# Kernel tuning notes

Hardware: AMD Instinct MI355X
Metric: run time of the kernel (lower is better)

## Reference

```python
import math
import jax, jax.numpy as jnp
import numpy as np

DIM = 512
HEADS = 8
HEAD_DIM = DIM // HEADS


def get_slopes(n):
    def pow2(n):
        start = 2 ** (-2 ** (-(math.log2(n) - 3)))
        return [start * start ** i for i in range(n)]
    if math.log2(n).is_integer():
        return pow2(n)
    c = 2 ** math.floor(math.log2(n))
    return pow2(c) + get_slopes(2 * c)[0::2][: n - c]


def setup_inputs() -> dict:
    key = jax.random.key(0)
    ks = jax.random.split(key, 12)
    b, n, d = 2, 4096, DIM
    s = 1.0 / math.sqrt(d)
    inp = {
        "x": jax.random.normal(ks[0], (b, n, d), jnp.float32),
        # coords in a ~[0,100) spatial range (tile grid coordinates)
        "coords": jax.random.uniform(ks[1], (b, n, 2), jnp.float32) * 100.0,
        "Wq": jax.random.normal(ks[2], (d, d), jnp.float32) * s,
        "bq": jnp.zeros((d,), jnp.float32),
        "Wk": jax.random.normal(ks[3], (d, d), jnp.float32) * s,
        "bk": jnp.zeros((d,), jnp.float32),
        "Wv": jax.random.normal(ks[4], (d, d), jnp.float32) * s,
        "bv": jnp.zeros((d,), jnp.float32),
        "Wp": jax.random.normal(ks[5], (d, d), jnp.float32) * s,
        "bp": jnp.zeros((d,), jnp.float32),
        "slopes": jnp.asarray(get_slopes(HEADS), jnp.float32),  # [h]
    }
    return inp


def reference(x, coords, Wq, bq, Wk, bk, Wv, bv, Wp, bp, slopes):
    b, n_q, d = x.shape
    h, hd = HEADS, HEAD_DIM
    # self-attention: context = x, context_coords = coords
    q = (x @ Wq + bq).reshape(b, n_q, h, hd).transpose(0, 2, 1, 3)  # b h nq hd
    k = (x @ Wk + bk).reshape(b, n_q, h, hd).transpose(0, 2, 1, 3)
    v = (x @ Wv + bv).reshape(b, n_q, h, hd).transpose(0, 2, 1, 3)
    # Euclidean-distance ALiBi bias: [b, h, nq, nk]
    diff = coords[:, :, None, :] - coords[:, None, :, :]          # b nq nk 2
    dist = jnp.sqrt(jnp.sum(diff * diff, axis=-1))                # b nq nk
    bias = -slopes[None, :, None, None] * dist[:, None, :, :]     # b h nq nk
    scores = jnp.einsum("bhqd,bhkd->bhqk", q, k) / math.sqrt(hd) + bias
    attn = jax.nn.softmax(scores, axis=-1)
    out = jnp.einsum("bhqk,bhkd->bhqd", attn, v)
    out = out.transpose(0, 2, 1, 3).reshape(b, n_q, d)
    return out @ Wp + bp
```

## Files before the change

### kernel.cpp

```cpp
#include <hip/hip_runtime.h>
#include <stdint.h>

typedef __bf16 bf16;
typedef __attribute__((ext_vector_type(8))) __bf16 bf16x8;
typedef __attribute__((ext_vector_type(4))) __bf16 bf16x4;
typedef __attribute__((ext_vector_type(4))) float f32x4;

#define DEVFN static __device__ __forceinline__

DEVFN void gload16(const bf16* g, char* l) {
  __builtin_amdgcn_global_load_lds(
      (const __attribute__((address_space(1))) void*)g,
      (__attribute__((address_space(3))) void*)l, 16, 0, 0);
}
DEVFN void gload4(const float* g, char* l) {
  __builtin_amdgcn_global_load_lds(
      (const __attribute__((address_space(1))) void*)g,
      (__attribute__((address_space(3))) void*)l, 4, 0, 0);
}

DEVFN int swz(int row, int kb) { return row * 128 + (kb ^ ((row & 7) << 4)); }

#define PS 9437184LL

__global__ __launch_bounds__(256) void prep_kernel(
    const float* __restrict__ x, const float* __restrict__ Wq,
    const float* __restrict__ Wk, const float* __restrict__ Wv,
    const float* __restrict__ Wp, bf16* __restrict__ xb,
    bf16* __restrict__ Wt, bf16* __restrict__ Wpt) {
  const int64_t tid = blockIdx.x * 256LL + threadIdx.x;
  const int64_t stride = (int64_t)gridDim.x * 256LL;
  for (int64_t i = tid; i < (8192LL * 512) / 4; i += stride) {
    float4 v = ((const float4*)x)[i];
    bf16x4 o = {(bf16)v.x, (bf16)v.y, (bf16)v.z, (bf16)v.w};
    ((bf16x4*)xb)[i] = o;
  }
  for (int64_t i = tid; i < 1536LL * 512; i += stride) {
    int c = (int)(i >> 9), k = (int)(i & 511);
    int wsel = c >> 9, cc = c & 511;
    const float* W = wsel == 0 ? Wq : (wsel == 1 ? Wk : Wv);
    Wt[i] = (bf16)W[k * 512 + cc];
  }
  for (int64_t i = tid; i < 512LL * 512; i += stride) {
    int c = (int)(i >> 9), k = (int)(i & 511);
    Wpt[i] = (bf16)Wp[k * 512 + c];
  }
}

DEVFN void gemm_main(const bf16* __restrict__ A, const bf16* __restrict__ B,
                     int rowA0, int rowB0, char* sA, char* sB, f32x4 acc[4][4],
                     int wr, int wc, int lane, int w) {
#pragma unroll
  for (int m = 0; m < 4; m++)
#pragma unroll
    for (int n = 0; n < 4; n++) acc[m][n] = (f32x4){0.f, 0.f, 0.f, 0.f};
  const int lr = lane >> 3;
  const int kswz = 8 * ((lane & 7) ^ lr);
  for (int k0 = 0; k0 < 512; k0 += 64) {
#pragma unroll
    for (int j = 0; j < 4; j++) {
      const int c = w * 4 + j;
      gload16(A + (rowA0 + c * 8 + lr) * 512 + k0 + kswz, sA + c * 1024);
      gload16(B + (rowB0 + c * 8 + lr) * 512 + k0 + kswz, sB + c * 1024);
    }
    __syncthreads();
    bf16x8 af[4][2], bfv[4][2];
#pragma unroll
    for (int m = 0; m < 4; m++)
#pragma unroll
      for (int kk = 0; kk < 2; kk++) {
        af[m][kk] = *(const bf16x8*)(sA + swz(wr * 64 + m * 16 + (lane & 15),
                                              kk * 64 + (lane >> 4) * 16));
        bfv[m][kk] = *(const bf16x8*)(sB + swz(wc * 64 + m * 16 + (lane & 15),
                                               kk * 64 + (lane >> 4) * 16));
      }
#pragma unroll
    for (int m = 0; m < 4; m++)
#pragma unroll
      for (int n = 0; n < 4; n++)
#pragma unroll
        for (int kk = 0; kk < 2; kk++)
          acc[m][n] = __builtin_amdgcn_mfma_f32_16x16x32_bf16(
              af[m][kk], bfv[n][kk], acc[m][n], 0, 0, 0);
    __syncthreads();
  }
}

__global__ __launch_bounds__(256) void qkv_gemm(
    const bf16* __restrict__ xb, const bf16* __restrict__ Wt,
    const float* __restrict__ bq, const float* __restrict__ bk,
    const float* __restrict__ bv, bf16* __restrict__ Qb, bf16* __restrict__ Kb,
    bf16* __restrict__ Vt) {
  __shared__ __align__(128) char sA[16384];
  __shared__ __align__(128) char sB[16384];
  const int lane = threadIdx.x & 63, w = threadIdx.x >> 6;
  const int wr = w >> 1, wc = w & 1;
  const int rowA0 = blockIdx.y * 128;
  const int colB0 = blockIdx.x * 128;
  f32x4 acc[4][4];
  gemm_main(xb, Wt, rowA0, colB0, sA, sB, acc, wr, wc, lane, w);
  const int which = colB0 >> 9;
  const int cc0 = colB0 & 511;
  const float* bias = which == 0 ? bq : (which == 1 ? bk : bv);
  const float QSCALE = 0.18033688011112042f;
#pragma unroll
  for (int m = 0; m < 4; m++)
#pragma unroll
    for (int n = 0; n < 4; n++)
#pragma unroll
      for (int r = 0; r < 4; r++) {
        int row = rowA0 + wr * 64 + m * 16 + (lane >> 4) * 4 + r;
        int col = cc0 + wc * 64 + n * 16 + (lane & 15);
        float v = acc[m][n][r] + bias[col];
        if (which == 0) {
          Qb[(int64_t)row * 512 + col] = (bf16)(v * QSCALE);
        } else if (which == 1) {
          Kb[(int64_t)row * 512 + col] = (bf16)v;
        } else {
          int b = row >> 12, nn = row & 4095;
          int hh = col >> 6, e = col & 63;
          Vt[(((int64_t)(b * 8 + hh)) * 64 + e) * 4096 + nn] = (bf16)v;
        }
      }
}

__global__ __launch_bounds__(256) void out_gemm(const bf16* __restrict__ Ob,
                                                const bf16* __restrict__ Wpt,
                                                const float* __restrict__ bp,
                                                float* __restrict__ out) {
  __shared__ __align__(128) char sA[16384];
  __shared__ __align__(128) char sB[16384];
  const int lane = threadIdx.x & 63, w = threadIdx.x >> 6;
  const int wr = w >> 1, wc = w & 1;
  const int rowA0 = blockIdx.y * 128;
  const int colB0 = blockIdx.x * 128;
  f32x4 acc[4][4];
  gemm_main(Ob, Wpt, rowA0, colB0, sA, sB, acc, wr, wc, lane, w);
#pragma unroll
  for (int m = 0; m < 4; m++)
#pragma unroll
    for (int n = 0; n < 4; n++)
#pragma unroll
      for (int r = 0; r < 4; r++) {
        int row = rowA0 + wr * 64 + m * 16 + (lane >> 4) * 4 + r;
        int col = colB0 + wc * 64 + n * 16 + (lane & 15);
        out[(int64_t)row * 512 + col] = acc[m][n][r] + bp[col];
      }
}

__global__ __launch_bounds__(512) void attn_kernel(
    const bf16* __restrict__ Qb, const bf16* __restrict__ Kb,
    const bf16* __restrict__ Vt, const float* __restrict__ coords,
    const float* __restrict__ slopes, char* __restrict__ part) {
  __shared__ __align__(128) char sK[2 * 8192];
  __shared__ __align__(128) char sV[2 * 8192];
  __shared__ __align__(128) char sC[2 * 512];
  __shared__ __align__(128) char sP[8 * 2048];

  const int tid = threadIdx.x;
  const int lane = tid & 63, w = tid >> 6;
  const int c = lane & 15, g = lane >> 4;

  const int id = blockIdx.x;
  const int bh = id & 15;
  const int qt = (id >> 4) & 31;
  const int ks = id >> 9;
  const int b = bh >> 3, h = bh & 7;
  const int qw = qt * 128 + w * 16;
  const int bO = b * 4096;
  const int kvs = ks * 2048;

  const float LOG2E = 1.4426950408889634f;
  const float negsl2 = -slopes[h] * LOG2E;

  bf16x8 aq[2];
  {
    int64_t base = ((int64_t)(bO + qw + c)) * 512 + h * 64 + g * 8;
    aq[0] = *(const bf16x8*)(Qb + base);
    aq[1] = *(const bf16x8*)(Qb + base + 32);
  }
  const float* cbf = coords + (int64_t)bO * 2;
  float qcx, qcy;
  {
    float2 qc = ((const float2*)cbf)[qw + c];
    qcx = qc.x;
    qcy = qc.y;
  }

  bf16x8 ones;
#pragma unroll
  for (int jj = 0; jj < 8; jj++) ones[jj] = (bf16)1.0f;

  float m2 = -1e30f;
  f32x4 o[4], osum;
#pragma unroll
  for (int n = 0; n < 4; n++) o[n] = (f32x4){0.f, 0.f, 0.f, 0.f};
  osum = (f32x4){0.f, 0.f, 0.f, 0.f};

  const bf16* Kp = Kb + (int64_t)bO * 512 + h * 64;
  const bf16* Vp = Vt + (int64_t)(b * 8 + h) * 262144;

  const int gi = w * 64 + lane;
  const int kr = gi >> 3, kj = gi & 7;
  const bf16* kq =
      Kp + (int64_t)(kvs + kr) * 512 + ((kj ^ (kr & 7)) * 8);
  const bf16* vq = Vp + kr * 4096 + kvs + ((kj ^ (kr & 7)) * 8);
  const float* cq = cbf + kvs * 2 + (w & 1) * 64 + lane;

  auto STAGE = [&](int bb) {
    gload16(kq, sK + bb * 8192 + gi * 16);
    kq += 64 * 512;
    gload16(vq, sV + bb * 8192 + gi * 16);
    vq += 64;
    if (w == 2 || w == 3) {
      gload4(cq, sC + bb * 512 + (w & 1) * 256);
      cq += 128;
    }
  };

  STAGE(0);
  __syncthreads();

  char* pwv = sP + w * 2048;
  const int cm = c & 7;
  for (int tt = 0; tt < 32; ++tt) {
    const int bb = tt & 1;
    if (tt + 1 < 32) STAGE(bb ^ 1);

    const char* kb = sK + bb * 8192;
    const char* vb = sV + bb * 8192;
    const char* cb0 = sC + bb * 512;

    bf16x8 kf[4][2];
#pragma unroll
    for (int t = 0; t < 4; t++)
#pragma unroll
      for (int kk = 0; kk < 2; kk++)
        kf[t][kk] = *(const bf16x8*)(kb + (t * 16 + c) * 128 +
                                     (((kk * 4 + g) ^ cm) * 16));
    float s[4][4];
    __builtin_amdgcn_s_setprio(1);
#pragma unroll
    for (int t = 0; t < 4; t++) {
      f32x4 sa = (f32x4){0.f, 0.f, 0.f, 0.f};
      sa = __builtin_amdgcn_mfma_f32_16x16x32_bf16(kf[t][0], aq[0], sa, 0, 0, 0);
      sa = __builtin_amdgcn_mfma_f32_16x16x32_bf16(kf[t][1], aq[1], sa, 0, 0, 0);
#pragma unroll
      for (int r = 0; r < 4; r++) s[t][r] = sa[r];
    }
    __builtin_amdgcn_s_setprio(0);

#pragma unroll
    for (int t = 0; t < 4; t++) {
      f32x4 ca = *(const f32x4*)(cb0 + 128 * t + 32 * g);
      f32x4 cb2 = *(const f32x4*)(cb0 + 128 * t + 32 * g + 16);
      float dx, dy;
#define DIST1(T, R, CX, CY)                                              \
  dx = qcx - (CX);                                                       \
  dy = qcy - (CY);                                                       \
  s[T][R] = __builtin_fmaf(__builtin_amdgcn_sqrtf(dx * dx + dy * dy),    \
                           negsl2, s[T][R]);
      DIST1(t, 0, ca[0], ca[1])
      DIST1(t, 1, ca[2], ca[3])
      DIST1(t, 2, cb2[0], cb2[1])
      DIST1(t, 3, cb2[2], cb2[3])
#undef DIST1
    }

    float lm = fmaxf(fmaxf(fmaxf(s[0][0], s[0][1]), fmaxf(s[0][2], s[0][3])),
                     fmaxf(fmaxf(s[1][0], s[1][1]), fmaxf(s[1][2], s[1][3])));
    lm = fmaxf(lm,
               fmaxf(fmaxf(fmaxf(s[2][0], s[2][1]), fmaxf(s[2][2], s[2][3])),
                     fmaxf(fmaxf(s[3][0], s[3][1]), fmaxf(s[3][2], s[3][3]))));
    if (__any(lm > m2 + 8.f)) {
      float lmf = fmaxf(lm, __shfl_xor(lm, 16));
      lmf = fmaxf(lmf, __shfl_xor(lmf, 32));
      float nm = fmaxf(m2, lmf);
      float sc = __builtin_amdgcn_exp2f(m2 - nm);
      m2 = nm;
      float scr[4];
#pragma unroll
      for (int r = 0; r < 4; r++)
        scr[r] = __shfl(sc, (lane & 48) | (4 * g + r));
#pragma unroll
      for (int n = 0; n < 4; n++)
#pragma unroll
        for (int r = 0; r < 4; r++) o[n][r] *= scr[r];
#pragma unroll
      for (int r = 0; r < 4; r++) osum[r] *= scr[r];
    }

#pragma unroll
    for (int t = 0; t < 4; t++) {
      bf16x4 pv = {(bf16)__builtin_amdgcn_exp2f(s[t][0] - m2),
                   (bf16)__builtin_amdgcn_exp2f(s[t][1] - m2),
                   (bf16)__builtin_amdgcn_exp2f(s[t][2] - m2),
                   (bf16)__builtin_amdgcn_exp2f(s[t][3] - m2)};
      *(bf16x4*)(pwv + c * 128 + (((2 * t + (g >> 1)) ^ cm) * 16) +
                 (g & 1) * 8) = pv;
    }
    bf16x8 pa0 = *(const bf16x8*)(pwv + c * 128 + ((g ^ cm) * 16));
    bf16x8 pa1 = *(const bf16x8*)(pwv + c * 128 + (((4 + g) ^ cm) * 16));

    __builtin_amdgcn_s_setprio(1);
#pragma unroll
    for (int n = 0; n < 4; n++) {
      const int e = n * 16 + c;
      bf16x8 vf0 = *(const bf16x8*)(vb + e * 128 + ((g ^ (e & 7)) * 16));
      bf16x8 vf1 = *(const bf16x8*)(vb + e * 128 + (((4 + g) ^ (e & 7)) * 16));
      o[n] = __builtin_amdgcn_mfma_f32_16x16x32_bf16(pa0, vf0, o[n], 0, 0, 0);
      o[n] = __builtin_amdgcn_mfma_f32_16x16x32_bf16(pa1, vf1, o[n], 0, 0, 0);
    }
    osum = __builtin_amdgcn_mfma_f32_16x16x32_bf16(pa0, ones, osum, 0, 0, 0);
    osum = __builtin_amdgcn_mfma_f32_16x16x32_bf16(pa1, ones, osum, 0, 0, 0);
    __builtin_amdgcn_s_setprio(0);

    __syncthreads();
  }

  float m2r[4];
#pragma unroll
  for (int r = 0; r < 4; r++)
    m2r[r] = __shfl(m2, (lane & 48) | (4 * g + r));
  char* pb0 = part + ks * PS + ((int64_t)bh * 4096 + qw) * 144;
#pragma unroll
  for (int r = 0; r < 4; r++) {
    char* pb = pb0 + (g * 4 + r) * 144;
    if (c == 0) {
      *(float*)pb = m2r[r];
      *((float*)pb + 1) = osum[r];
    }
#pragma unroll
    for (int n = 0; n < 4; n++)
      *(bf16*)(pb + 16 + (n * 16 + c) * 2) = (bf16)o[n][r];
  }
}

__global__ __launch_bounds__(256) void combine_kernel(
    const char* __restrict__ part, bf16* __restrict__ Ob) {
  const int t = blockIdx.x * 256 + threadIdx.x;
  const int row = t >> 6;
  const int e = t & 63;
  const char* p0 = part + (int64_t)row * 144;
  const char* p1 = p0 + PS;
  const float m0 = *(const float*)p0, s0 = *((const float*)p0 + 1);
  const float m1 = *(const float*)p1, s1 = *((const float*)p1 + 1);
  const float o0 = (float)*(const bf16*)(p0 + 16 + e * 2);
  const float o1 = (float)*(const bf16*)(p1 + 16 + e * 2);
  const float m = fmaxf(m0, m1);
  const float w0 = __builtin_amdgcn_exp2f(m0 - m);
  const float w1 = __builtin_amdgcn_exp2f(m1 - m);
  const float res = (o0 * w0 + o1 * w1) / (s0 * w0 + s1 * w1);
  const int bh = row >> 12, q = row & 4095;
  Ob[((int64_t)((bh >> 3) * 4096 + q)) * 512 + (bh & 7) * 64 + e] = (bf16)res;
}

extern "C" void kernel_launch(void* const* d_in, const int* in_sizes, int n_in,
                              void* d_out, int out_size, void* d_ws,
                              size_t ws_size, hipStream_t stream) {
  const float* x = (const float*)d_in[0];
  const float* coords = (const float*)d_in[1];
  const float* Wq = (const float*)d_in[2];
  const float* bq = (const float*)d_in[3];
  const float* Wk = (const float*)d_in[4];
  const float* bk = (const float*)d_in[5];
  const float* Wv = (const float*)d_in[6];
  const float* bv = (const float*)d_in[7];
  const float* Wp = (const float*)d_in[8];
  const float* bp = (const float*)d_in[9];
  const float* slopes = (const float*)d_in[10];

  char* ws = (char*)d_ws;
  bf16* xb = (bf16*)(ws);
  bf16* Wt = (bf16*)(ws + 8388608);
  bf16* Wpt = (bf16*)(ws + 9961472);
  bf16* Qb = (bf16*)(ws + 10485760);
  bf16* Kb = (bf16*)(ws + 18874368);
  bf16* Vt = (bf16*)(ws + 27262976);
  bf16* Ob = (bf16*)(ws + 35651584);
  char* part = ws + 44040192;

  hipLaunchKernelGGL(prep_kernel, dim3(1024), dim3(256), 0, stream, x, Wq, Wk,
                     Wv, Wp, xb, Wt, Wpt);
  hipLaunchKernelGGL(qkv_gemm, dim3(12, 64), dim3(256), 0, stream, xb, Wt, bq,
                     bk, bv, Qb, Kb, Vt);
  hipLaunchKernelGGL(attn_kernel, dim3(1024), dim3(512), 0, stream, Qb, Kb,
                     Vt, coords, slopes, part);
  hipLaunchKernelGGL(combine_kernel, dim3(16384), dim3(256), 0, stream, part,
                     Ob);
  hipLaunchKernelGGL(out_gemm, dim3(4, 64), dim3(256), 0, stream, Ob, Wpt, bp,
                     (float*)d_out);
}
```

Measured before the change: 215.1 us.

## Process two 16-row query sub-tiles per wave to reuse K/V fragments

Each wave now handles 32 query rows (two 16-row sub-tiles) instead of 16, so every K and V fragment loaded from LDS feeds twice as many MFMAs, and each block covers 256 queries. The grid is halved to 512 blocks, which cuts K/V global traffic and staging per query. In exchange, register pressure roughly doubles for accumulators and scores, and fewer blocks (512 on a GPU with 256 CUs) may reduce occupancy and latency hiding. The per-wave P scratch buffer is reused serially for both sub-tiles, which adds an LDS write/read dependency.

```diff
diff --git a/kernel.cpp b/kernel.cpp
--- a/kernel.cpp
+++ b/kernel.cpp
@@ -163,47 +163,49 @@
 
   const int id = blockIdx.x;
   const int bh = id & 15;
-  const int qt = (id >> 4) & 31;
-  const int ks = id >> 9;
+  const int qt = (id >> 4) & 15;
+  const int ks = id >> 8;
   const int b = bh >> 3, h = bh & 7;
-  const int qw = qt * 128 + w * 16;
+  const int qw = qt * 256 + w * 32;
   const int bO = b * 4096;
   const int kvs = ks * 2048;
 
   const float LOG2E = 1.4426950408889634f;
   const float negsl2 = -slopes[h] * LOG2E;
 
-  bf16x8 aq[2];
-  {
-    int64_t base = ((int64_t)(bO + qw + c)) * 512 + h * 64 + g * 8;
-    aq[0] = *(const bf16x8*)(Qb + base);
-    aq[1] = *(const bf16x8*)(Qb + base + 32);
-  }
+  bf16x8 aq[2][2];
+  float qcx[2], qcy[2];
   const float* cbf = coords + (int64_t)bO * 2;
-  float qcx, qcy;
-  {
-    float2 qc = ((const float2*)cbf)[qw + c];
-    qcx = qc.x;
-    qcy = qc.y;
+#pragma unroll
+  for (int s2 = 0; s2 < 2; s2++) {
+    int64_t base =
+        ((int64_t)(bO + qw + s2 * 16 + c)) * 512 + h * 64 + g * 8;
+    aq[s2][0] = *(const bf16x8*)(Qb + base);
+    aq[s2][1] = *(const bf16x8*)(Qb + base + 32);
+    float2 qc = ((const float2*)cbf)[qw + s2 * 16 + c];
+    qcx[s2] = qc.x;
+    qcy[s2] = qc.y;
   }
 
   bf16x8 ones;
 #pragma unroll
   for (int jj = 0; jj < 8; jj++) ones[jj] = (bf16)1.0f;
 
-  float m2 = -1e30f;
-  f32x4 o[4], osum;
-#pragma unroll
-  for (int n = 0; n < 4; n++) o[n] = (f32x4){0.f, 0.f, 0.f, 0.f};
-  osum = (f32x4){0.f, 0.f, 0.f, 0.f};
+  float m2[2] = {-1e30f, -1e30f};
+  f32x4 o[2][4], osum[2];
+#pragma unroll
+  for (int s2 = 0; s2 < 2; s2++) {
+#pragma unroll
+    for (int n = 0; n < 4; n++) o[s2][n] = (f32x4){0.f, 0.f, 0.f, 0.f};
+    osum[s2] = (f32x4){0.f, 0.f, 0.f, 0.f};
+  }
 
   const bf16* Kp = Kb + (int64_t)bO * 512 + h * 64;
   const bf16* Vp = Vt + (int64_t)(b * 8 + h) * 262144;
 
   const int gi = w * 64 + lane;
   const int kr = gi >> 3, kj = gi & 7;
-  const bf16* kq =
-      Kp + (int64_t)(kvs + kr) * 512 + ((kj ^ (kr & 7)) * 8);
+  const bf16* kq = Kp + (int64_t)(kvs + kr) * 512 + ((kj ^ (kr & 7)) * 8);
   const bf16* vq = Vp + kr * 4096 + kvs + ((kj ^ (kr & 7)) * 8);
   const float* cq = cbf + kvs * 2 + (w & 1) * 64 + lane;
 
@@ -238,69 +240,81 @@
       for (int kk = 0; kk < 2; kk++)
         kf[t][kk] = *(const bf16x8*)(kb + (t * 16 + c) * 128 +
                                      (((kk * 4 + g) ^ cm) * 16));
-    float s[4][4];
+    float s[2][4][4];
     __builtin_amdgcn_s_setprio(1);
 #pragma unroll
-    for (int t = 0; t < 4; t++) {
-      f32x4 sa = (f32x4){0.f, 0.f, 0.f, 0.f};
-      sa = __builtin_amdgcn_mfma_f32_16x16x32_bf16(kf[t][0], aq[0], sa, 0, 0, 0);
-      sa = __builtin_amdgcn_mfma_f32_16x16x32_bf16(kf[t][1], aq[1], sa, 0, 0, 0);
-#pragma unroll
-      for (int r = 0; r < 4; r++) s[t][r] = sa[r];
-    }
+    for (int s2 = 0; s2 < 2; s2++)
+#pragma unroll
+      for (int t = 0; t < 4; t++) {
+        f32x4 sa = (f32x4){0.f, 0.f, 0.f, 0.f};
+        sa = __builtin_amdgcn_mfma_f32_16x16x32_bf16(kf[t][0], aq[s2][0], sa,
+                                                     0, 0, 0);
+        sa = __builtin_amdgcn_mfma_f32_16x16x32_bf16(kf[t][1], aq[s2][1], sa,
+                                                     0, 0, 0);
+#pragma unroll
+        for (int r = 0; r < 4; r++) s[s2][t][r] = sa[r];
+      }
     __builtin_amdgcn_s_setprio(0);
 
-#pragma unroll
-    for (int t = 0; t < 4; t++) {
-      f32x4 ca = *(const f32x4*)(cb0 + 128 * t + 32 * g);
-      f32x4 cb2 = *(const f32x4*)(cb0 + 128 * t + 32 * g + 16);
-      float dx, dy;
-#define DIST1(T, R, CX, CY)                                              \
-  dx = qcx - (CX);                                                       \
-  dy = qcy - (CY);                                                       \
-  s[T][R] = __builtin_fmaf(__builtin_amdgcn_sqrtf(dx * dx + dy * dy),    \
-                           negsl2, s[T][R]);
-      DIST1(t, 0, ca[0], ca[1])
-      DIST1(t, 1, ca[2], ca[3])
-      DIST1(t, 2, cb2[0], cb2[1])
-      DIST1(t, 3, cb2[2], cb2[3])
+    bf16x8 pa[2][2];
+#pragma unroll
+    for (int s2 = 0; s2 < 2; s2++) {
+#pragma unroll
+      for (int t = 0; t < 4; t++) {
+        f32x4 ca = *(const f32x4*)(cb0 + 128 * t + 32 * g);
+        f32x4 cb2 = *(const f32x4*)(cb0 + 128 * t + 32 * g + 16);
+        float dx, dy;
+#define DIST1(T, R, CX, CY)                                                \
+  dx = qcx[s2] - (CX);                                                     \
+  dy = qcy[s2] - (CY);                                                     \
+  s[s2][T][R] = __builtin_fmaf(                                            \
+      __builtin_amdgcn_sqrtf(dx * dx + dy * dy), negsl2, s[s2][T][R]);
+        DIST1(t, 0, ca[0], ca[1])
+        DIST1(t, 1, ca[2], ca[3])
+        DIST1(t, 2, cb2[0], cb2[1])
+        DIST1(t, 3, cb2[2], cb2[3])
 #undef DIST1
-    }
-
-    float lm = fmaxf(fmaxf(fmaxf(s[0][0], s[0][1]), fmaxf(s[0][2], s[0][3])),
-                     fmaxf(fmaxf(s[1][0], s[1][1]), fmaxf(s[1][2], s[1][3])));
-    lm = fmaxf(lm,
-               fmaxf(fmaxf(fmaxf(s[2][0], s[2][1]), fmaxf(s[2][2], s[2][3])),
-                     fmaxf(fmaxf(s[3][0], s[3][1]), fmaxf(s[3][2], s[3][3]))));
-    if (__any(lm > m2 + 8.f)) {
-      float lmf = fmaxf(lm, __shfl_xor(lm, 16));
-      lmf = fmaxf(lmf, __shfl_xor(lmf, 32));
-      float nm = fmaxf(m2, lmf);
-      float sc = __builtin_amdgcn_exp2f(m2 - nm);
-      m2 = nm;
-      float scr[4];
-#pragma unroll
-      for (int r = 0; r < 4; r++)
-        scr[r] = __shfl(sc, (lane & 48) | (4 * g + r));
-#pragma unroll
-      for (int n = 0; n < 4; n++)
-#pragma unroll
-        for (int r = 0; r < 4; r++) o[n][r] *= scr[r];
-#pragma unroll
-      for (int r = 0; r < 4; r++) osum[r] *= scr[r];
-    }
-
-#pragma unroll
-    for (int t = 0; t < 4; t++) {
-      bf16x4 pv = {(bf16)__builtin_amdgcn_exp2f(s[t][0] - m2),
-                   (bf16)__builtin_amdgcn_exp2f(s[t][1] - m2),
-                   (bf16)__builtin_amdgcn_exp2f(s[t][2] - m2),
-                   (bf16)__builtin_amdgcn_exp2f(s[t][3] - m2)};
-      *(bf16x4*)(pwv + c * 128 + (((2 * t + (g >> 1)) ^ cm) * 16) +
-                 (g & 1) * 8) = pv;
-    }
-    bf16x8 pa0 = *(const bf16x8*)(pwv + c * 128 + ((g ^ cm) * 16));
-    bf16x8 pa1 = *(const bf16x8*)(pwv + c * 128 + (((4 + g) ^ cm) * 16));
+      }
+
+      float lm = fmaxf(
+          fmaxf(fmaxf(s[s2][0][0], s[s2][0][1]), fmaxf(s[s2][0][2], s[s2][0][3])),
+          fmaxf(fmaxf(s[s2][1][0], s[s2][1][1]), fmaxf(s[s2][1][2], s[s2][1][3])));
+      lm = fmaxf(
+          lm,
+          fmaxf(fmaxf(fmaxf(s[s2][2][0], s[s2][2][1]),
+                      fmaxf(s[s2][2][2], s[s2][2][3])),
+                fmaxf(fmaxf(s[s2][3][0], s[s2][3][1]),
+                      fmaxf(s[s2][3][2], s[s2][3][3]))));
+      if (__any(lm > m2[s2] + 8.f)) {
+        float lmf = fmaxf(lm, __shfl_xor(lm, 16));
+        lmf = fmaxf(lmf, __shfl_xor(lmf, 32));
+        float nm = fmaxf(m2[s2], lmf);
+        float sc = __builtin_amdgcn_exp2f(m2[s2] - nm);
+        m2[s2] = nm;
+        float scr[4];
+#pragma unroll
+        for (int r = 0; r < 4; r++)
+          scr[r] = __shfl(sc, (lane & 48) | (4 * g + r));
+#pragma unroll
+        for (int n = 0; n < 4; n++)
+#pragma unroll
+          for (int r = 0; r < 4; r++) o[s2][n][r] *= scr[r];
+#pragma unroll
+        for (int r = 0; r < 4; r++) osum[s2][r] *= scr[r];
+      }
+
+#pragma unroll
+      for (int t = 0; t < 4; t++) {
+        bf16x4 pv = {(bf16)__builtin_amdgcn_exp2f(s[s2][t][0] - m2[s2]),
+                     (bf16)__builtin_amdgcn_exp2f(s[s2][t][1] - m2[s2]),
+                     (bf16)__builtin_amdgcn_exp2f(s[s2][t][2] - m2[s2]),
+                     (bf16)__builtin_amdgcn_exp2f(s[s2][t][3] - m2[s2])};
+        *(bf16x4*)(pwv + c * 128 + (((2 * t + (g >> 1)) ^ cm) * 16) +
+                   (g & 1) * 8) = pv;
+      }
+      pa[s2][0] = *(const bf16x8*)(pwv + c * 128 + ((g ^ cm) * 16));
+      pa[s2][1] = *(const bf16x8*)(pwv + c * 128 + (((4 + g) ^ cm) * 16));
+    }
 
     __builtin_amdgcn_s_setprio(1);
 #pragma unroll
@@ -308,31 +322,47 @@
       const int e = n * 16 + c;
       bf16x8 vf0 = *(const bf16x8*)(vb + e * 128 + ((g ^ (e & 7)) * 16));
       bf16x8 vf1 = *(const bf16x8*)(vb + e * 128 + (((4 + g) ^ (e & 7)) * 16));
-      o[n] = __builtin_amdgcn_mfma_f32_16x16x32_bf16(pa0, vf0, o[n], 0, 0, 0);
-      o[n] = __builtin_amdgcn_mfma_f32_16x16x32_bf16(pa1, vf1, o[n], 0, 0, 0);
-    }
-    osum = __builtin_amdgcn_mfma_f32_16x16x32_bf16(pa0, ones, osum, 0, 0, 0);
-    osum = __builtin_amdgcn_mfma_f32_16x16x32_bf16(pa1, ones, osum, 0, 0, 0);
+#pragma unroll
+      for (int s2 = 0; s2 < 2; s2++) {
+        o[s2][n] =
+            __builtin_amdgcn_mfma_f32_16x16x32_bf16(pa[s2][0], vf0, o[s2][n],
+                                                    0, 0, 0);
+        o[s2][n] =
+            __builtin_amdgcn_mfma_f32_16x16x32_bf16(pa[s2][1], vf1, o[s2][n],
+                                                    0, 0, 0);
+      }
+    }
+#pragma unroll
+    for (int s2 = 0; s2 < 2; s2++) {
+      osum[s2] = __builtin_amdgcn_mfma_f32_16x16x32_bf16(pa[s2][0], ones,
+                                                         osum[s2], 0, 0, 0);
+      osum[s2] = __builtin_amdgcn_mfma_f32_16x16x32_bf16(pa[s2][1], ones,
+                                                         osum[s2], 0, 0, 0);
+    }
     __builtin_amdgcn_s_setprio(0);
 
     __syncthreads();
   }
 
-  float m2r[4];
-#pragma unroll
-  for (int r = 0; r < 4; r++)
-    m2r[r] = __shfl(m2, (lane & 48) | (4 * g + r));
-  char* pb0 = part + ks * PS + ((int64_t)bh * 4096 + qw) * 144;
-#pragma unroll
-  for (int r = 0; r < 4; r++) {
-    char* pb = pb0 + (g * 4 + r) * 144;
-    if (c == 0) {
-      *(float*)pb = m2r[r];
-      *((float*)pb + 1) = osum[r];
-    }
-#pragma unroll
-    for (int n = 0; n < 4; n++)
-      *(bf16*)(pb + 16 + (n * 16 + c) * 2) = (bf16)o[n][r];
+#pragma unroll
+  for (int s2 = 0; s2 < 2; s2++) {
+    float m2r[4];
+#pragma unroll
+    for (int r = 0; r < 4; r++)
+      m2r[r] = __shfl(m2[s2], (lane & 48) | (4 * g + r));
+    char* pb0 =
+        part + ks * PS + ((int64_t)bh * 4096 + qw + s2 * 16) * 144;
+#pragma unroll
+    for (int r = 0; r < 4; r++) {
+      char* pb = pb0 + (g * 4 + r) * 144;
+      if (c == 0) {
+        *(float*)pb = m2r[r];
+        *((float*)pb + 1) = osum[s2][r];
+      }
+#pragma unroll
+      for (int n = 0; n < 4; n++)
+        *(bf16*)(pb + 16 + (n * 16 + c) * 2) = (bf16)o[s2][n][r];
+    }
   }
 }
 
@@ -384,7 +414,7 @@
                      Wv, Wp, xb, Wt, Wpt);
   hipLaunchKernelGGL(qkv_gemm, dim3(12, 64), dim3(256), 0, stream, xb, Wt, bq,
                      bk, bv, Qb, Kb, Vt);
-  hipLaunchKernelGGL(attn_kernel, dim3(1024), dim3(512), 0, stream, Qb, Kb,
+  hipLaunchKernelGGL(attn_kernel, dim3(512), dim3(512), 0, stream, Qb, Kb,
                      Vt, coords, slopes, part);
   hipLaunchKernelGGL(combine_kernel, dim3(16384), dim3(256), 0, stream, part,
                      Ob);
```

After: 233.5 us. 8.6% more time.

## Permute K rows to keep P in registers and vectorize combine kernel

Applied to the files above, without the earlier changes.

K rows are loaded into shared memory in a permuted order, and the coordinate reads are remapped to match. This lets the softmax probabilities from the QK^T MFMA output be fed straight into the PV MFMA as register operands, removing the per-wave LDS write/read round trip for P. The combine kernel also changes to process eight output elements per thread with 16-byte loads and stores, using a reciprocal instead of per-element division, and launches correspondingly fewer blocks. The risk is in the index mapping: the permutation has to match the K, V and coordinate orderings consistently.

```diff
diff --git a/kernel.cpp b/kernel.cpp
--- a/kernel.cpp
+++ b/kernel.cpp
@@ -155,7 +155,6 @@
   __shared__ __align__(128) char sK[2 * 8192];
   __shared__ __align__(128) char sV[2 * 8192];
   __shared__ __align__(128) char sC[2 * 512];
-  __shared__ __align__(128) char sP[8 * 2048];
 
   const int tid = threadIdx.x;
   const int lane = tid & 63, w = tid >> 6;
@@ -202,8 +201,9 @@
 
   const int gi = w * 64 + lane;
   const int kr = gi >> 3, kj = gi & 7;
-  const bf16* kq =
-      Kp + (int64_t)(kvs + kr) * 512 + ((kj ^ (kr & 7)) * 8);
+  const int pkr = ((kr >> 4) & 1) * 32 + ((kr >> 2) & 3) * 8 +
+                  ((kr >> 5) & 1) * 4 + (kr & 3);
+  const bf16* kq = Kp + (int64_t)(kvs + pkr) * 512 + ((kj ^ (kr & 7)) * 8);
   const bf16* vq = Vp + kr * 4096 + kvs + ((kj ^ (kr & 7)) * 8);
   const float* cq = cbf + kvs * 2 + (w & 1) * 64 + lane;
 
@@ -221,7 +221,6 @@
   STAGE(0);
   __syncthreads();
 
-  char* pwv = sP + w * 2048;
   const int cm = c & 7;
   for (int tt = 0; tt < 32; ++tt) {
     const int bb = tt & 1;
@@ -252,8 +251,9 @@
 
 #pragma unroll
     for (int t = 0; t < 4; t++) {
-      f32x4 ca = *(const f32x4*)(cb0 + 128 * t + 32 * g);
-      f32x4 cb2 = *(const f32x4*)(cb0 + 128 * t + 32 * g + 16);
+      const int cbo = (t & 1) * 256 + (t >> 1) * 32 + g * 64;
+      f32x4 ca = *(const f32x4*)(cb0 + cbo);
+      f32x4 cb2 = *(const f32x4*)(cb0 + cbo + 16);
       float dx, dy;
 #define DIST1(T, R, CX, CY)                                              \
   dx = qcx - (CX);                                                       \
@@ -290,17 +290,14 @@
       for (int r = 0; r < 4; r++) osum[r] *= scr[r];
     }
 
-#pragma unroll
-    for (int t = 0; t < 4; t++) {
-      bf16x4 pv = {(bf16)__builtin_amdgcn_exp2f(s[t][0] - m2),
-                   (bf16)__builtin_amdgcn_exp2f(s[t][1] - m2),
-                   (bf16)__builtin_amdgcn_exp2f(s[t][2] - m2),
-                   (bf16)__builtin_amdgcn_exp2f(s[t][3] - m2)};
-      *(bf16x4*)(pwv + c * 128 + (((2 * t + (g >> 1)) ^ cm) * 16) +
-                 (g & 1) * 8) = pv;
-    }
-    bf16x8 pa0 = *(const bf16x8*)(pwv + c * 128 + ((g ^ cm) * 16));
-    bf16x8 pa1 = *(const bf16x8*)(pwv + c * 128 + (((4 + g) ^ cm) * 16));
+    bf16x8 pa0, pa1;
+#pragma unroll
+    for (int r = 0; r < 4; r++) {
+      pa0[r] = (bf16)__builtin_amdgcn_exp2f(s[0][r] - m2);
+      pa0[4 + r] = (bf16)__builtin_amdgcn_exp2f(s[2][r] - m2);
+      pa1[r] = (bf16)__builtin_amdgcn_exp2f(s[1][r] - m2);
+      pa1[4 + r] = (bf16)__builtin_amdgcn_exp2f(s[3][r] - m2);
+    }
 
     __builtin_amdgcn_s_setprio(1);
 #pragma unroll
@@ -339,20 +336,25 @@
 __global__ __launch_bounds__(256) void combine_kernel(
     const char* __restrict__ part, bf16* __restrict__ Ob) {
   const int t = blockIdx.x * 256 + threadIdx.x;
-  const int row = t >> 6;
-  const int e = t & 63;
+  const int row = t >> 3;
+  const int eb = (t & 7) * 8;
   const char* p0 = part + (int64_t)row * 144;
   const char* p1 = p0 + PS;
   const float m0 = *(const float*)p0, s0 = *((const float*)p0 + 1);
   const float m1 = *(const float*)p1, s1 = *((const float*)p1 + 1);
-  const float o0 = (float)*(const bf16*)(p0 + 16 + e * 2);
-  const float o1 = (float)*(const bf16*)(p1 + 16 + e * 2);
+  bf16x8 o0 = *(const bf16x8*)(p0 + 16 + eb * 2);
+  bf16x8 o1 = *(const bf16x8*)(p1 + 16 + eb * 2);
   const float m = fmaxf(m0, m1);
   const float w0 = __builtin_amdgcn_exp2f(m0 - m);
   const float w1 = __builtin_amdgcn_exp2f(m1 - m);
-  const float res = (o0 * w0 + o1 * w1) / (s0 * w0 + s1 * w1);
+  const float inv = 1.f / (s0 * w0 + s1 * w1);
+  bf16x8 res;
+#pragma unroll
+  for (int j = 0; j < 8; j++)
+    res[j] = (bf16)(((float)o0[j] * w0 + (float)o1[j] * w1) * inv);
   const int bh = row >> 12, q = row & 4095;
-  Ob[((int64_t)((bh >> 3) * 4096 + q)) * 512 + (bh & 7) * 64 + e] = (bf16)res;
+  *(bf16x8*)(Ob + ((int64_t)((bh >> 3) * 4096 + q)) * 512 + (bh & 7) * 64 +
+             eb) = res;
 }
 
 extern "C" void kernel_launch(void* const* d_in, const int* in_sizes, int n_in,
@@ -386,7 +388,7 @@
                      bk, bv, Qb, Kb, Vt);
   hipLaunchKernelGGL(attn_kernel, dim3(1024), dim3(512), 0, stream, Qb, Kb,
                      Vt, coords, slopes, part);
-  hipLaunchKernelGGL(combine_kernel, dim3(16384), dim3(256), 0, stream, part,
+  hipLaunchKernelGGL(combine_kernel, dim3(2048), dim3(256), 0, stream, part,
                      Ob);
   hipLaunchKernelGGL(out_gemm, dim3(4, 64), dim3(256), 0, stream, Ob, Wpt, bp,
                      (float*)d_out);
```

After: 210.7 us. -2.0%, faster.
